# Kernel optimization log

Hardware: AMD Instinct MI355X
Metric: run time of the kernel (lower is better)

## Reference

```python
import jax, jax.numpy as jnp
import numpy as np

DIM = 512
HEADS = 8
HEAD_DIM = 64
RS = 16        # region_size
EPEG_K = 15
L_TOKENS = 36864  # 192^2, multiple of RS^2 grid


def setup_inputs() -> dict:
    key = jax.random.key(0)
    ks = jax.random.split(key, 5)
    s = 1.0 / np.sqrt(DIM)
    x = jax.random.normal(ks[0], (1, L_TOKENS, DIM), jnp.float32)
    W_qkv = jax.random.normal(ks[1], (3 * HEADS * HEAD_DIM, DIM), jnp.float32) * s
    b_qkv = jnp.zeros((3 * HEADS * HEAD_DIM,), jnp.float32)
    W_proj = jax.random.normal(ks[2], (DIM, HEADS * HEAD_DIM), jnp.float32) * s
    b_proj = jnp.zeros((DIM,), jnp.float32)
    pe_w = jax.random.normal(ks[3], (HEADS, 1, EPEG_K, 1), jnp.float32) * 0.05
    pe_b = jnp.zeros((HEADS,), jnp.float32)
    return dict(x=x, W_qkv=W_qkv, b_qkv=b_qkv, W_proj=W_proj, b_proj=b_proj,
                pe_w=pe_w, pe_b=pe_b)


def reference(x, W_qkv, b_qkv, W_proj, b_proj, pe_w, pe_b):
    B, L, C = x.shape
    # --- padding() logic: square to HxW, H multiple of region_size ---
    H = int(np.ceil(np.sqrt(L)))
    H += (-H) % RS
    W = H
    add = H * W - L
    if add > 0:
        x = jnp.concatenate([x, jnp.zeros((B, add, C), x.dtype)], axis=1)
    # --- region_partition: (B,H,W,C) -> (num_regions*B, RS*RS, C) ---
    xr = (x.reshape(B, H // RS, RS, W // RS, RS, C)
            .transpose(0, 1, 3, 2, 4, 5)
            .reshape(-1, RS * RS, C))
    B_, N, _ = xr.shape
    # --- InnerAttention ---
    qkv = xr @ W_qkv.T + b_qkv                       # (B_, N, 3*h*d)
    qkv = qkv.reshape(B_, N, 3, HEADS, HEAD_DIM).transpose(2, 0, 3, 1, 4)
    q, k, v = qkv[0], qkv[1], qkv[2]                 # each (B_, h, N, d)
    scale = HEAD_DIM ** -0.5
    attn = jnp.einsum('bhid,bhjd->bhij', q * scale, k)   # (B_, h, N, N)
    # EPEG: depthwise conv (k,1) over the query axis of the score map
    pad = EPEG_K // 2
    pe = jax.lax.conv_general_dilated(
        attn, pe_w, window_strides=(1, 1), padding=((pad, pad), (0, 0)),
        dimension_numbers=('NCHW', 'OIHW', 'NCHW'), feature_group_count=HEADS)
    pe = pe + pe_b[None, :, None, None]
    attn = jax.nn.softmax(attn + pe, axis=-1)
    out = jnp.einsum('bhij,bhjd->bhid', attn, v)     # (B_, h, N, d)
    out = out.transpose(0, 2, 1, 3).reshape(B_, N, HEADS * HEAD_DIM)
    out = out @ W_proj.T + b_proj                    # (B_, N, C)
    # --- region_reverse ---
    out = (out.reshape(B, H // RS, W // RS, RS, RS, C)
              .transpose(0, 1, 3, 2, 4, 5)
              .reshape(B, H * W, C))
    if add > 0:
        out = out[:, :L]
    return out
```

## Files before the change

### kernel.cpp

```cpp
#include <hip/hip_runtime.h>
#include <stdint.h>

typedef __attribute__((ext_vector_type(8))) __bf16 bf16x8;
typedef __attribute__((ext_vector_type(16))) float f32x16;

__device__ __forceinline__ unsigned short f2bf(float f) {
  union { float f; unsigned int u; } v;
  v.f = f;
  unsigned int u = v.u;
  return (unsigned short)((u + 0x7FFFu + ((u >> 16) & 1u)) >> 16);
}

union BFrag { unsigned short u[8]; unsigned int w[4]; bf16x8 v; };

__device__ __forceinline__ f32x16 mfma32(bf16x8 a, bf16x8 b, f32x16 c) {
  return __builtin_amdgcn_mfma_f32_32x32x16_bf16(a, b, c, 0, 0, 0);
}

#define GLOAD_LDS16(gptr, lptr)                                                \
  __builtin_amdgcn_global_load_lds(                                           \
      (const __attribute__((address_space(1))) void*)(gptr),                  \
      (__attribute__((address_space(3))) void*)(lptr), 16, 0, 0)

__global__ __launch_bounds__(256) void k_xgather(const float* __restrict__ x,
                                                 unsigned short* __restrict__ xb) {
  int idx = blockIdx.x * 256 + threadIdx.x;
  int m = idx >> 6;
  int seg = (idx & 63) << 3;
  int r = m >> 8, n = m & 255;
  int a = r / 12, b = r - a * 12;
  int ii = n >> 4, jj = n & 15;
  long g = (long)((a * 16 + ii) * 192 + b * 16 + jj);
  const float4* p = (const float4*)(x + g * 512 + seg);
  float4 v0 = p[0], v1 = p[1];
  union { unsigned short u[8]; int4 v; } o;
  o.u[0] = f2bf(v0.x); o.u[1] = f2bf(v0.y); o.u[2] = f2bf(v0.z); o.u[3] = f2bf(v0.w);
  o.u[4] = f2bf(v1.x); o.u[5] = f2bf(v1.y); o.u[6] = f2bf(v1.z); o.u[7] = f2bf(v1.w);
  *(int4*)(xb + (size_t)m * 512 + seg) = o.v;
}

__global__ __launch_bounds__(256) void k_cvt(const float* __restrict__ s,
                                             unsigned short* __restrict__ d, int n8) {
  int i = blockIdx.x * 256 + threadIdx.x;
  if (i >= n8) return;
  const float4* p = (const float4*)(s + (size_t)i * 8);
  float4 a = p[0], b = p[1];
  union { unsigned short u[8]; int4 v; } o;
  o.u[0] = f2bf(a.x); o.u[1] = f2bf(a.y); o.u[2] = f2bf(a.z); o.u[3] = f2bf(a.w);
  o.u[4] = f2bf(b.x); o.u[5] = f2bf(b.y); o.u[6] = f2bf(b.z); o.u[7] = f2bf(b.w);
  *(int4*)(d + (size_t)i * 8) = o.v;
}

template<int MODE, int NBN>
__global__ __launch_bounds__(256, 2) void k_gemm(
    const unsigned short* __restrict__ A, const unsigned short* __restrict__ B,
    const float* __restrict__ bias,
    unsigned short* __restrict__ qb, unsigned short* __restrict__ kb,
    unsigned short* __restrict__ vtb, float* __restrict__ out) {
  __shared__ unsigned short As[8192];
  __shared__ unsigned short Bs[8192];
  int t = threadIdx.x;
  constexpr int NWG = NBN * 288;
  int d0 = blockIdx.x;
  int tl = (d0 & 7) * (NWG >> 3) + (d0 >> 3);
  int bm = tl / NBN, bn = tl % NBN;

  int w = t >> 6, lane = t & 63;
  int l31 = lane & 31, lh = lane >> 5;
  int wr = w >> 1, wc = w & 1;

  int srow = t >> 3, cseg = t & 7;
  int csw = (cseg ^ (srow & 7)) << 3;
  int ldsWaveOff = (t >> 6) << 10;

  f32x16 acc[2][2];
  for (int i = 0; i < 2; ++i)
    for (int j = 0; j < 2; ++j)
      for (int e = 0; e < 16; ++e) acc[i][j][e] = 0.0f;

  const unsigned short* Ag = A + (size_t)(bm * 128 + srow) * 512 + csw;
  const unsigned short* Bg = B + (size_t)(bn * 128 + srow) * 512 + csw;

  for (int ks = 0; ks < 8; ++ks) {
#pragma unroll
    for (int rnd = 0; rnd < 4; ++rnd) {
      GLOAD_LDS16(Ag + (size_t)rnd * 32 * 512 + ks * 64,
                  (char*)As + ldsWaveOff + rnd * 4096);
      GLOAD_LDS16(Bg + (size_t)rnd * 32 * 512 + ks * 64,
                  (char*)Bs + ldsWaveOff + rnd * 4096);
    }
    __syncthreads();
#pragma unroll
    for (int kt = 0; kt < 4; ++kt) {
      bf16x8 af[2], bfr[2];
#pragma unroll
      for (int mt = 0; mt < 2; ++mt) {
        int r = wr * 64 + mt * 32 + l31;
        af[mt] = *(const bf16x8*)((const char*)As + r * 128 +
                                  ((kt * 32 + lh * 16) ^ ((r & 7) << 4)));
      }
#pragma unroll
      for (int nt = 0; nt < 2; ++nt) {
        int r = wc * 64 + nt * 32 + l31;
        bfr[nt] = *(const bf16x8*)((const char*)Bs + r * 128 +
                                   ((kt * 32 + lh * 16) ^ ((r & 7) << 4)));
      }
#pragma unroll
      for (int mt = 0; mt < 2; ++mt)
#pragma unroll
        for (int nt = 0; nt < 2; ++nt)
          acc[mt][nt] = mfma32(af[mt], bfr[nt], acc[mt][nt]);
    }
    __syncthreads();
  }

  int nBase = bn * 128 + wc * 64;
  int mBase = bm * 128 + wr * 64;
#pragma unroll
  for (int nt = 0; nt < 2; ++nt) {
    int nn = nBase + nt * 32 + l31;
    float bs = bias[nn];
    if (MODE == 0) {
      int tsel = nn >> 9, rem = nn & 511;
      int hh = rem >> 6, d = rem & 63;
#pragma unroll
      for (int mt = 0; mt < 2; ++mt) {
#pragma unroll
        for (int q = 0; q < 4; ++q) {
          int m0 = mBase + mt * 32 + q * 8 + lh * 4;
          int r = m0 >> 8, tok = m0 & 255;
          size_t base = (size_t)(r * 8 + hh) * 16384;
          if (tsel == 0) {
#pragma unroll
            for (int j = 0; j < 4; ++j)
              qb[base + (size_t)(tok + j) * 64 + d] = f2bf((acc[mt][nt][q * 4 + j] + bs) * 0.125f);
          } else if (tsel == 1) {
#pragma unroll
            for (int j = 0; j < 4; ++j)
              kb[base + (size_t)(tok + j) * 64 + d] = f2bf(acc[mt][nt][q * 4 + j] + bs);
          } else {
            unsigned long long pv = 0;
#pragma unroll
            for (int j = 0; j < 4; ++j)
              pv |= (unsigned long long)f2bf(acc[mt][nt][q * 4 + j] + bs) << (16 * j);
            *(unsigned long long*)(vtb + base + (size_t)d * 256 + tok) = pv;
          }
        }
      }
    } else {
#pragma unroll
      for (int mt = 0; mt < 2; ++mt) {
#pragma unroll
        for (int q = 0; q < 4; ++q) {
          int m0 = mBase + mt * 32 + q * 8 + lh * 4;
          int r = m0 >> 8;
          int a = r / 12, bcol = r - a * 12;
#pragma unroll
          for (int j = 0; j < 4; ++j) {
            int tok = (m0 & 255) + j;
            int ii = tok >> 4, jj = tok & 15;
            long gg = (long)((a * 16 + ii) * 192 + bcol * 16 + jj);
            out[gg * 512 + nn] = acc[mt][nt][q * 4 + j] + bs;
          }
        }
      }
    }
  }
}

__global__ __launch_bounds__(512, 2) void k_attn(
    const unsigned short* __restrict__ qb, const unsigned short* __restrict__ kb,
    const unsigned short* __restrict__ vtb, const float* __restrict__ pe_w,
    unsigned short* __restrict__ ctxb) {
  extern __shared__ char lds[];
  int rh = blockIdx.x;
  int h = rh & 7;
  int t = threadIdx.x, w = t >> 6, lane = t & 63;
  int l31 = lane & 31, lh = lane >> 5;
  int qi = (w << 5) + l31;

  const unsigned short* Qg = qb + (size_t)rh * 16384;
  const unsigned short* Kg = kb + (size_t)rh * 16384;
  const unsigned short* Vg = vtb + (size_t)rh * 16384;

#pragma unroll
  for (int p = 0; p < 4; ++p) {
    int c = p * 512 + t;
    int row = c >> 3, cc = c & 7;
    int4 vq = *(const int4*)(Qg + (size_t)row * 64 + cc * 8);
    int4 vk = *(const int4*)(Kg + (size_t)row * 64 + cc * 8);
    int so = row * 128 + ((cc ^ (row & 7)) << 4);
    *(int4*)(lds + so) = vq;
    *(int4*)(lds + 32768 + so) = vk;
  }
#pragma unroll
  for (int p = 0; p < 4; ++p) {
    int c = p * 512 + t;
    int row = c >> 5, cc = c & 31;
    int4 vv = *(const int4*)(Vg + (size_t)row * 256 + cc * 8);
    *(int4*)(lds + 131072 + row * 512 + ((cc ^ (row & 7)) << 4)) = vv;
  }
  __syncthreads();

  f32x16 acc[8];
#pragma unroll
  for (int mt = 0; mt < 8; ++mt)
    for (int e = 0; e < 16; ++e) acc[mt][e] = 0.0f;

  bf16x8 bq[4];
#pragma unroll
  for (int kt = 0; kt < 4; ++kt)
    bq[kt] = *(const bf16x8*)(lds + (qi * 128 + (((kt * 2 + lh) ^ (qi & 7)) << 4)));

#pragma unroll
  for (int mt = 0; mt < 8; ++mt) {
    int kj = (mt << 5) + l31;
    int rb = 32768 + kj * 128;
#pragma unroll
    for (int kt = 0; kt < 4; ++kt) {
      bf16x8 ak = *(const bf16x8*)(lds + (rb + (((kt * 2 + lh) ^ (kj & 7)) << 4)));
      acc[mt] = mfma32(ak, bq[kt], acc[mt]);
    }
  }
  __syncthreads();

#pragma unroll
  for (int mt = 0; mt < 8; ++mt) {
#pragma unroll
    for (int rg = 0; rg < 16; ++rg) {
      int j = (mt << 5) + (rg & 3) + ((rg >> 2) << 3) + (lh << 2);
      int byte = (j * 512 + qi * 2) ^ ((j & 7) << 4);
      *(unsigned short*)(lds + byte) = f2bf(acc[mt][rg]);
    }
  }
  __syncthreads();

  const float* wh = pe_w + h * 15;
#pragma unroll
  for (int kt4 = 0; kt4 < 4; ++kt4) {
    int ktg = 2 * w - 1 + kt4;
    if (ktg >= 0 && ktg <= 15) {
      BFrag bb;
#pragma unroll
      for (int e = 0; e < 8; ++e) {
        int ip = (ktg << 4) + (lh << 3) + e;
        int diff = ip - qi + 7;
        float val = (diff >= 0 && diff <= 14) ? wh[diff] : 0.0f;
        bb.u[e] = f2bf(val);
      }
#pragma unroll
      for (int mt = 0; mt < 8; ++mt) {
        int j = (mt << 5) + l31;
        int byte = (j * 512 + (ktg << 5) + (lh << 4)) ^ ((j & 7) << 4);
        bf16x8 aa = *(const bf16x8*)(lds + byte);
        acc[mt] = mfma32(aa, bb.v, acc[mt]);
      }
    }
  }

  float mx = -3.0e38f;
#pragma unroll
  for (int mt = 0; mt < 8; ++mt)
#pragma unroll
    for (int e = 0; e < 16; ++e) mx = fmaxf(mx, acc[mt][e]);
  mx = fmaxf(mx, __shfl_xor(mx, 32));
  float sum = 0.0f;
#pragma unroll
  for (int mt = 0; mt < 8; ++mt)
#pragma unroll
    for (int e = 0; e < 16; ++e) {
      float pp = __expf(acc[mt][e] - mx);
      acc[mt][e] = pp;
      sum += pp;
    }
  sum += __shfl_xor(sum, 32);
  float inv = 1.0f / sum;

  f32x16 acco[2];
  for (int nt = 0; nt < 2; ++nt)
    for (int e = 0; e < 16; ++e) acco[nt][e] = 0.0f;

#pragma unroll
  for (int mt = 0; mt < 8; ++mt) {
    unsigned int pk[8], sw[8];
#pragma unroll
    for (int u = 0; u < 8; ++u) {
      float lo = acc[mt][2 * u] * inv, hi = acc[mt][2 * u + 1] * inv;
      pk[u] = (unsigned int)f2bf(lo) | ((unsigned int)f2bf(hi) << 16);
    }
#pragma unroll
    for (int u = 0; u < 8; ++u) sw[u] = (unsigned int)__shfl_xor((int)pk[u], 32);
    BFrag f0, f1;
    if (lh == 0) {
      f0.w[0] = pk[0]; f0.w[1] = pk[1]; f0.w[2] = sw[0]; f0.w[3] = sw[1];
      f1.w[0] = pk[4]; f1.w[1] = pk[5]; f1.w[2] = sw[4]; f1.w[3] = sw[5];
    } else {
      f0.w[0] = sw[2]; f0.w[1] = sw[3]; f0.w[2] = pk[2]; f0.w[3] = pk[3];
      f1.w[0] = sw[6]; f1.w[1] = sw[7]; f1.w[2] = pk[6]; f1.w[3] = pk[7];
    }
#pragma unroll
    for (int nt = 0; nt < 2; ++nt) {
      int d = (nt << 5) + l31;
      int base = 131072 + d * 512;
      bf16x8 bv0 = *(const bf16x8*)(lds + base + (((mt << 6) + (lh << 4)) ^ ((d & 7) << 4)));
      bf16x8 bv1 = *(const bf16x8*)(lds + base + (((mt << 6) + 32 + (lh << 4)) ^ ((d & 7) << 4)));
      acco[nt] = mfma32(f0.v, bv0, acco[nt]);
      acco[nt] = mfma32(f1.v, bv1, acco[nt]);
    }
  }

  int r = rh >> 3;
#pragma unroll
  for (int nt = 0; nt < 2; ++nt) {
    int d = h * 64 + (nt << 5) + l31;
#pragma unroll
    for (int rg = 0; rg < 16; ++rg) {
      int i = (w << 5) + (rg & 3) + ((rg >> 2) << 3) + (lh << 2);
      ctxb[(size_t)(r * 256 + i) * 512 + d] = f2bf(acco[nt][rg]);
    }
  }
}

extern "C" void kernel_launch(void* const* d_in, const int* in_sizes, int n_in,
                              void* d_out, int out_size, void* d_ws, size_t ws_size,
                              hipStream_t stream) {
  const float* x = (const float*)d_in[0];
  const float* Wqkv = (const float*)d_in[1];
  const float* bqkv = (const float*)d_in[2];
  const float* Wproj = (const float*)d_in[3];
  const float* bproj = (const float*)d_in[4];
  const float* pew = (const float*)d_in[5];

  char* ws = (char*)d_ws;
  unsigned short* xb = (unsigned short*)ws;
  unsigned short* wqkvb = (unsigned short*)(ws + 37748736);
  unsigned short* wprojb = (unsigned short*)(ws + 39321600);
  unsigned short* qb = (unsigned short*)(ws + 39845888);
  unsigned short* kb = (unsigned short*)(ws + 77594624);
  unsigned short* vtb = (unsigned short*)(ws + 115343360);

  (void)hipFuncSetAttribute((const void*)k_attn,
                            hipFuncAttributeMaxDynamicSharedMemorySize, 163840);

  k_xgather<<<9216, 256, 0, stream>>>(x, xb);
  k_cvt<<<384, 256, 0, stream>>>(Wqkv, wqkvb, 98304);
  k_cvt<<<128, 256, 0, stream>>>(Wproj, wprojb, 32768);
  k_gemm<0, 12><<<3456, 256, 0, stream>>>(xb, wqkvb, bqkv, qb, kb, vtb, nullptr);
  k_attn<<<1152, 512, 163840, stream>>>(qb, kb, vtb, pew, xb);
  k_gemm<1, 4><<<1152, 256, 0, stream>>>(xb, wprojb, bproj, nullptr, nullptr, nullptr,
                                         (float*)d_out);
}
```

Measured before the change: 222.5 us.

## Restructure attention kernel into tiled online-softmax with reduced LDS footprint

The attention kernel is rewritten to use 256 threads, each wave handling 64 queries, with the key dimension processed in four 64-wide tiles using online softmax. K and V tiles are loaded with direct global-to-LDS loads, Q fragments are kept in registers, and the EPEG band weights are precomputed once into LDS. This cuts the LDS requirement from 160KB to about 72KB so more blocks can be resident and load latency can overlap compute. In exchange it adds per-tile barriers, rescaling work, and a per-tile transpose of scores through LDS for the conv MFMA.

Result: slower. 385.8 us (+73.4%).

```diff
diff --git a/kernel.cpp b/kernel.cpp
--- a/kernel.cpp
+++ b/kernel.cpp
@@ -168,7 +168,7 @@
   }
 }
 
-__global__ __launch_bounds__(512, 2) void k_attn(
+__global__ __launch_bounds__(256, 2) void k_attn2(
     const unsigned short* __restrict__ qb, const unsigned short* __restrict__ kb,
     const unsigned short* __restrict__ vtb, const float* __restrict__ pe_w,
     unsigned short* __restrict__ ctxb) {
@@ -177,148 +177,205 @@
   int h = rh & 7;
   int t = threadIdx.x, w = t >> 6, lane = t & 63;
   int l31 = lane & 31, lh = lane >> 5;
-  int qi = (w << 5) + l31;
+  int iw = w << 6;
 
   const unsigned short* Qg = qb + (size_t)rh * 16384;
   const unsigned short* Kg = kb + (size_t)rh * 16384;
   const unsigned short* Vg = vtb + (size_t)rh * 16384;
-
-#pragma unroll
-  for (int p = 0; p < 4; ++p) {
-    int c = p * 512 + t;
-    int row = c >> 3, cc = c & 7;
-    int4 vq = *(const int4*)(Qg + (size_t)row * 64 + cc * 8);
-    int4 vk = *(const int4*)(Kg + (size_t)row * 64 + cc * 8);
-    int so = row * 128 + ((cc ^ (row & 7)) << 4);
-    *(int4*)(lds + so) = vq;
-    *(int4*)(lds + 32768 + so) = vk;
+  const float* wh = pe_w + h * 15;
+
+#pragma unroll
+  for (int rr = 0; rr < 8; ++rr) {
+    int row = rr * 32 + (t >> 3);
+    GLOAD_LDS16(Kg + row * 64 + (((t & 7) ^ (row & 7)) << 3), lds + rr * 4096 + t * 16);
   }
-#pragma unroll
-  for (int p = 0; p < 4; ++p) {
-    int c = p * 512 + t;
-    int row = c >> 5, cc = c & 31;
-    int4 vv = *(const int4*)(Vg + (size_t)row * 256 + cc * 8);
-    *(int4*)(lds + 131072 + row * 512 + ((cc ^ (row & 7)) << 4)) = vv;
+  if (t < 96) {
+    int dlo = t - 40, dhi = t - 39;
+    unsigned int lo = (dlo >= 0 && dlo < 15) ? f2bf(wh[dlo]) : 0;
+    unsigned int hi = (dhi >= 0 && dhi < 15) ? f2bf(wh[dhi]) : 0;
+    *(unsigned int*)(lds + 73728 + t * 4) = lo | (hi << 16);
   }
+  bf16x8 qf[2][4];
+#pragma unroll
+  for (int ib = 0; ib < 2; ++ib)
+#pragma unroll
+    for (int kt = 0; kt < 4; ++kt)
+      qf[ib][kt] = *(const bf16x8*)(Qg + (size_t)(iw + ib * 32 + l31) * 64 + kt * 16 + lh * 8);
   __syncthreads();
 
-  f32x16 acc[8];
-#pragma unroll
-  for (int mt = 0; mt < 8; ++mt)
-    for (int e = 0; e < 16; ++e) acc[mt][e] = 0.0f;
-
-  bf16x8 bq[4];
-#pragma unroll
-  for (int kt = 0; kt < 4; ++kt)
-    bq[kt] = *(const bf16x8*)(lds + (qi * 128 + (((kt * 2 + lh) ^ (qi & 7)) << 4)));
-
-#pragma unroll
-  for (int mt = 0; mt < 8; ++mt) {
-    int kj = (mt << 5) + l31;
-    int rb = 32768 + kj * 128;
-#pragma unroll
-    for (int kt = 0; kt < 4; ++kt) {
-      bf16x8 ak = *(const bf16x8*)(lds + (rb + (((kt * 2 + lh) ^ (kj & 7)) << 4)));
-      acc[mt] = mfma32(ak, bq[kt], acc[mt]);
+  BFrag band[2][4];
+#pragma unroll
+  for (int ib = 0; ib < 2; ++ib)
+#pragma unroll
+    for (int u = 0; u < 4; ++u) {
+      int ktg = 4 * w + 2 * ib + u - 1;
+      if (ktg >= 0 && ktg < 16) {
+        int d0 = ktg * 16 + lh * 8 - (iw + ib * 32 + l31) + 47;
+#pragma unroll
+        for (int e2 = 0; e2 < 4; ++e2)
+          band[ib][u].w[e2] = *(const unsigned int*)(lds + 73728 + (d0 + 2 * e2) * 4);
+      } else {
+        band[ib][u].w[0] = band[ib][u].w[1] = band[ib][u].w[2] = band[ib][u].w[3] = 0;
+      }
+    }
+
+  float m[2] = {-3.0e38f, -3.0e38f}, l[2] = {0.0f, 0.0f};
+  f32x16 acco[2][2];
+#pragma unroll
+  for (int ib = 0; ib < 2; ++ib)
+#pragma unroll
+    for (int nt = 0; nt < 2; ++nt)
+#pragma unroll
+      for (int e = 0; e < 16; ++e) acco[ib][nt][e] = 0.0f;
+
+#pragma unroll
+  for (int tile = 0; tile < 4; ++tile) {
+    f32x16 sacc[2][2];
+#pragma unroll
+    for (int jb = 0; jb < 2; ++jb)
+#pragma unroll
+      for (int ib = 0; ib < 2; ++ib)
+#pragma unroll
+        for (int e = 0; e < 16; ++e) sacc[jb][ib][e] = 0.0f;
+#pragma unroll
+    for (int jb = 0; jb < 2; ++jb) {
+      int kr = tile * 64 + jb * 32 + l31;
+#pragma unroll
+      for (int kt = 0; kt < 4; ++kt) {
+        bf16x8 kf = *(const bf16x8*)(lds + kr * 128 + (((kt * 2 + lh) ^ (kr & 7)) << 4));
+        sacc[jb][0] = mfma32(kf, qf[0][kt], sacc[jb][0]);
+        sacc[jb][1] = mfma32(kf, qf[1][kt], sacc[jb][1]);
+      }
+    }
+    __syncthreads();
+
+#pragma unroll
+    for (int rr = 0; rr < 2; ++rr) {
+      int row = rr * 32 + (t >> 3);
+      GLOAD_LDS16(Vg + row * 256 + tile * 64 + (((t & 7) ^ (row & 7)) << 3),
+                  lds + 65536 + rr * 4096 + t * 16);
+    }
+
+#pragma unroll
+    for (int jb = 0; jb < 2; ++jb)
+#pragma unroll
+      for (int ib = 0; ib < 2; ++ib) {
+        int i2 = (iw + ib * 32 + l31) * 2;
+#pragma unroll
+        for (int rg = 0; rg < 16; ++rg) {
+          int j = jb * 32 + (rg & 3) + 8 * (rg >> 2) + 4 * lh;
+          *(unsigned short*)(lds + 32768 + j * 512 + (i2 ^ ((j & 7) << 4))) =
+              f2bf(sacc[jb][ib][rg]);
+        }
+      }
+    __syncthreads();
+
+#pragma unroll
+    for (int jb = 0; jb < 2; ++jb) {
+      int jr = jb * 32 + l31;
+      bf16x8 sfr[6];
+#pragma unroll
+      for (int ci = 0; ci < 6; ++ci) {
+        int ktg = 4 * w + ci - 1;
+        if (ktg >= 0 && ktg < 16)
+          sfr[ci] = *(const bf16x8*)(lds + 32768 + jr * 512 +
+                                     ((ktg * 32 + lh * 16) ^ ((jr & 7) << 4)));
+      }
+#pragma unroll
+      for (int ib = 0; ib < 2; ++ib)
+#pragma unroll
+        for (int u = 0; u < 4; ++u) {
+          int ktg = 4 * w + 2 * ib + u - 1;
+          if (ktg >= 0 && ktg < 16)
+            sacc[jb][ib] = mfma32(sfr[2 * ib + u], band[ib][u].v, sacc[jb][ib]);
+        }
+    }
+
+    float fct[2];
+#pragma unroll
+    for (int ib = 0; ib < 2; ++ib) {
+      float pm = -3.0e38f;
+#pragma unroll
+      for (int jb = 0; jb < 2; ++jb)
+#pragma unroll
+        for (int e = 0; e < 16; ++e) pm = fmaxf(pm, sacc[jb][ib][e]);
+      pm = fmaxf(pm, __shfl_xor(pm, 32));
+      float mn = fmaxf(m[ib], pm);
+      float f = __expf(m[ib] - mn);
+      fct[ib] = f;
+      float ts = 0.0f;
+#pragma unroll
+      for (int jb = 0; jb < 2; ++jb)
+#pragma unroll
+        for (int e = 0; e < 16; ++e) {
+          float p = __expf(sacc[jb][ib][e] - mn);
+          sacc[jb][ib][e] = p;
+          ts += p;
+        }
+      ts += __shfl_xor(ts, 32);
+      l[ib] = (tile == 0) ? ts : l[ib] * f + ts;
+      m[ib] = mn;
+    }
+    if (tile != 0) {
+#pragma unroll
+      for (int ib = 0; ib < 2; ++ib)
+#pragma unroll
+        for (int rg = 0; rg < 16; ++rg) {
+          float g = __shfl(fct[ib], (rg & 3) + 8 * (rg >> 2) + 4 * lh);
+          acco[ib][0][rg] *= g;
+          acco[ib][1][rg] *= g;
+        }
+    }
+
+#pragma unroll
+    for (int jb = 0; jb < 2; ++jb) {
+      BFrag pf[2][2];
+#pragma unroll
+      for (int ib = 0; ib < 2; ++ib) {
+        unsigned int pk[8], sw[8];
+#pragma unroll
+        for (int u = 0; u < 8; ++u)
+          pk[u] = (unsigned int)f2bf(sacc[jb][ib][2 * u]) |
+                  ((unsigned int)f2bf(sacc[jb][ib][2 * u + 1]) << 16);
+#pragma unroll
+        for (int u = 0; u < 8; ++u) sw[u] = (unsigned int)__shfl_xor((int)pk[u], 32);
+        if (lh == 0) {
+          pf[ib][0].w[0] = pk[0]; pf[ib][0].w[1] = pk[1]; pf[ib][0].w[2] = sw[0]; pf[ib][0].w[3] = sw[1];
+          pf[ib][1].w[0] = pk[4]; pf[ib][1].w[1] = pk[5]; pf[ib][1].w[2] = sw[4]; pf[ib][1].w[3] = sw[5];
+        } else {
+          pf[ib][0].w[0] = sw[2]; pf[ib][0].w[1] = sw[3]; pf[ib][0].w[2] = pk[2]; pf[ib][0].w[3] = pk[3];
+          pf[ib][1].w[0] = sw[6]; pf[ib][1].w[1] = sw[7]; pf[ib][1].w[2] = pk[6]; pf[ib][1].w[3] = pk[7];
+        }
+      }
+#pragma unroll
+      for (int nt = 0; nt < 2; ++nt) {
+        int vr = nt * 32 + l31;
+#pragma unroll
+        for (int kj2 = 0; kj2 < 2; ++kj2) {
+          int kj = jb * 2 + kj2;
+          bf16x8 vf = *(const bf16x8*)(lds + 65536 + vr * 128 +
+                                       (((kj * 2 + lh) ^ (vr & 7)) << 4));
+          acco[0][nt] = mfma32(pf[0][kj2].v, vf, acco[0][nt]);
+          acco[1][nt] = mfma32(pf[1][kj2].v, vf, acco[1][nt]);
+        }
+      }
     }
   }
-  __syncthreads();
-
-#pragma unroll
-  for (int mt = 0; mt < 8; ++mt) {
+
+  float inv[2] = {1.0f / l[0], 1.0f / l[1]};
+  int r256 = (rh >> 3) * 256;
+  int chbase = h * 64;
+#pragma unroll
+  for (int ib = 0; ib < 2; ++ib)
 #pragma unroll
     for (int rg = 0; rg < 16; ++rg) {
-      int j = (mt << 5) + (rg & 3) + ((rg >> 2) << 3) + (lh << 2);
-      int byte = (j * 512 + qi * 2) ^ ((j & 7) << 4);
-      *(unsigned short*)(lds + byte) = f2bf(acc[mt][rg]);
-    }
-  }
-  __syncthreads();
-
-  const float* wh = pe_w + h * 15;
-#pragma unroll
-  for (int kt4 = 0; kt4 < 4; ++kt4) {
-    int ktg = 2 * w - 1 + kt4;
-    if (ktg >= 0 && ktg <= 15) {
-      BFrag bb;
-#pragma unroll
-      for (int e = 0; e < 8; ++e) {
-        int ip = (ktg << 4) + (lh << 3) + e;
-        int diff = ip - qi + 7;
-        float val = (diff >= 0 && diff <= 14) ? wh[diff] : 0.0f;
-        bb.u[e] = f2bf(val);
-      }
-#pragma unroll
-      for (int mt = 0; mt < 8; ++mt) {
-        int j = (mt << 5) + l31;
-        int byte = (j * 512 + (ktg << 5) + (lh << 4)) ^ ((j & 7) << 4);
-        bf16x8 aa = *(const bf16x8*)(lds + byte);
-        acc[mt] = mfma32(aa, bb.v, acc[mt]);
-      }
-    }
-  }
-
-  float mx = -3.0e38f;
-#pragma unroll
-  for (int mt = 0; mt < 8; ++mt)
-#pragma unroll
-    for (int e = 0; e < 16; ++e) mx = fmaxf(mx, acc[mt][e]);
-  mx = fmaxf(mx, __shfl_xor(mx, 32));
-  float sum = 0.0f;
-#pragma unroll
-  for (int mt = 0; mt < 8; ++mt)
-#pragma unroll
-    for (int e = 0; e < 16; ++e) {
-      float pp = __expf(acc[mt][e] - mx);
-      acc[mt][e] = pp;
-      sum += pp;
-    }
-  sum += __shfl_xor(sum, 32);
-  float inv = 1.0f / sum;
-
-  f32x16 acco[2];
-  for (int nt = 0; nt < 2; ++nt)
-    for (int e = 0; e < 16; ++e) acco[nt][e] = 0.0f;
-
-#pragma unroll
-  for (int mt = 0; mt < 8; ++mt) {
-    unsigned int pk[8], sw[8];
-#pragma unroll
-    for (int u = 0; u < 8; ++u) {
-      float lo = acc[mt][2 * u] * inv, hi = acc[mt][2 * u + 1] * inv;
-      pk[u] = (unsigned int)f2bf(lo) | ((unsigned int)f2bf(hi) << 16);
-    }
-#pragma unroll
-    for (int u = 0; u < 8; ++u) sw[u] = (unsigned int)__shfl_xor((int)pk[u], 32);
-    BFrag f0, f1;
-    if (lh == 0) {
-      f0.w[0] = pk[0]; f0.w[1] = pk[1]; f0.w[2] = sw[0]; f0.w[3] = sw[1];
-      f1.w[0] = pk[4]; f1.w[1] = pk[5]; f1.w[2] = sw[4]; f1.w[3] = sw[5];
-    } else {
-      f0.w[0] = sw[2]; f0.w[1] = sw[3]; f0.w[2] = pk[2]; f0.w[3] = pk[3];
-      f1.w[0] = sw[6]; f1.w[1] = sw[7]; f1.w[2] = pk[6]; f1.w[3] = pk[7];
-    }
-#pragma unroll
-    for (int nt = 0; nt < 2; ++nt) {
-      int d = (nt << 5) + l31;
-      int base = 131072 + d * 512;
-      bf16x8 bv0 = *(const bf16x8*)(lds + base + (((mt << 6) + (lh << 4)) ^ ((d & 7) << 4)));
-      bf16x8 bv1 = *(const bf16x8*)(lds + base + (((mt << 6) + 32 + (lh << 4)) ^ ((d & 7) << 4)));
-      acco[nt] = mfma32(f0.v, bv0, acco[nt]);
-      acco[nt] = mfma32(f1.v, bv1, acco[nt]);
-    }
-  }
-
-  int r = rh >> 3;
-#pragma unroll
-  for (int nt = 0; nt < 2; ++nt) {
-    int d = h * 64 + (nt << 5) + l31;
-#pragma unroll
-    for (int rg = 0; rg < 16; ++rg) {
-      int i = (w << 5) + (rg & 3) + ((rg >> 2) << 3) + (lh << 2);
-      ctxb[(size_t)(r * 256 + i) * 512 + d] = f2bf(acco[nt][rg]);
-    }
-  }
+      int cr = (rg & 3) + 8 * (rg >> 2) + 4 * lh;
+      float g = __shfl(inv[ib], cr);
+      int i = iw + ib * 32 + cr;
+      size_t rowoff = (size_t)(r256 + i) * 512 + chbase;
+      ctxb[rowoff + l31] = f2bf(acco[ib][0][rg] * g);
+      ctxb[rowoff + 32 + l31] = f2bf(acco[ib][1][rg] * g);
+    }
 }
 
 extern "C" void kernel_launch(void* const* d_in, const int* in_sizes, int n_in,
@@ -339,14 +396,14 @@
   unsigned short* kb = (unsigned short*)(ws + 77594624);
   unsigned short* vtb = (unsigned short*)(ws + 115343360);
 
-  (void)hipFuncSetAttribute((const void*)k_attn,
+  (void)hipFuncSetAttribute((const void*)k_attn2,
                             hipFuncAttributeMaxDynamicSharedMemorySize, 163840);
 
   k_xgather<<<9216, 256, 0, stream>>>(x, xb);
   k_cvt<<<384, 256, 0, stream>>>(Wqkv, wqkvb, 98304);
   k_cvt<<<128, 256, 0, stream>>>(Wproj, wprojb, 32768);
   k_gemm<0, 12><<<3456, 256, 0, stream>>>(xb, wqkvb, bqkv, qb, kb, vtb, nullptr);
-  k_attn<<<1152, 512, 163840, stream>>>(qb, kb, vtb, pew, xb);
+  k_attn2<<<1152, 256, 74112, stream>>>(qb, kb, vtb, pew, xb);
   k_gemm<1, 4><<<1152, 256, 0, stream>>>(xb, wprojb, bproj, nullptr, nullptr, nullptr,
                                          (float*)d_out);
 }
```
